# Performance work log

Hardware: AMD Instinct MI355X
Metric: run time of the kernel (lower is better)

The kernel has to match this reference:

```python
import jax, jax.numpy as jnp
import numpy as np
import math

N, LQ, D, H, L, P, DFF, NL = 16, 300, 256, 8, 3, 4, 1024, 6
TLENS = (4096, 2048, 1024)
T = sum(TLENS)
TEMP = 10000.0

def _ln(x, g, b, eps=1e-5):
    m = x.mean(-1, keepdims=True)
    v = ((x - m) ** 2).mean(-1, keepdims=True)
    return (x - m) * jax.lax.rsqrt(v + eps) * g + b

def _mlp2(x, w0, b0, w1, b1):
    return jax.nn.relu(x @ w0.T + b0) @ w1.T + b1

def _sine_embed(ref):
    # ref: (N, LQ, 2) (center, width) -> (N, LQ, 2*D)
    dim_t = TEMP ** (2.0 * (jnp.arange(D) // 2) / D)
    p = ref * (2.0 * math.pi)
    def inter(v):
        return jnp.stack([jnp.sin(v[..., 0::2]), jnp.cos(v[..., 1::2])], -1).reshape(v.shape[:-1] + (-1,))
    pc = p[..., 0:1] / dim_t
    pw = p[..., 1:2] / dim_t
    return jnp.concatenate([inter(pc), inter(pw)], -1)

def _mha(q, k, v, in_w, in_b, out_w, out_b):
    Nb, Lq, Dm = q.shape
    Dh = Dm // H
    wq, wk, wv = jnp.split(in_w, 3, 0)
    bq, bk, bv = jnp.split(in_b, 3, 0)
    qh = (q @ wq.T + bq).reshape(Nb, Lq, H, Dh)
    kh = (k @ wk.T + bk).reshape(Nb, Lq, H, Dh)
    vh = (v @ wv.T + bv).reshape(Nb, Lq, H, Dh)
    att = jax.nn.softmax(jnp.einsum('nqhd,nkhd->nhqk', qh, kh) / math.sqrt(Dh), -1)
    o = jnp.einsum('nhqk,nkhd->nqhd', att, vh).reshape(Nb, Lq, Dm)
    return o @ out_w.T + out_b

def _deform_attn(q, ref, src, pad_mask, t_lens, start, ow, ob, aww, awb, vw, vb, pw, pb):
    # q: (N,LQ,D); ref: (N,LQ,L,2) normalized (center,width); src: (N,T,D)
    Nb, Lq, Dm = q.shape
    Dh = Dm // H
    val = (src @ vw.T + vb) * (~pad_mask)[..., None]
    val = val.reshape(Nb, -1, H, Dh).transpose(0, 2, 1, 3)  # (N,H,T,Dh)
    off = (q @ ow.T + ob).reshape(Nb, Lq, H, L, P)
    aw = jax.nn.softmax((q @ aww.T + awb).reshape(Nb, Lq, H, L * P), -1).reshape(Nb, Lq, H, L, P)
    # 1-D deformable sampling locations: center + offset/P * width * 0.5
    loc = ref[:, :, None, :, 0, None] + off / P * ref[:, :, None, :, 1, None] * 0.5  # (N,LQ,H,L,P)
    tl = t_lens[None, None, None, :, None]
    x = loc * tl.astype(loc.dtype) - 0.5  # align_corners=False linear sampling
    x0f = jnp.floor(x)
    f = x - x0f
    x0 = x0f.astype(jnp.int32)
    m0 = (x0 >= 0) & (x0 < tl)
    m1 = (x0 + 1 >= 0) & (x0 + 1 < tl)
    st = start[None, None, None, :, None]
    i0 = st + jnp.clip(x0, 0, tl - 1)
    i1 = st + jnp.clip(x0 + 1, 0, tl - 1)
    def tr(a):
        return a.transpose(0, 2, 1, 3, 4).reshape(Nb, H, Lq * L * P)
    g0 = jnp.take_along_axis(val, tr(i0)[..., None], axis=2)  # (N,H,M,Dh)
    g1 = jnp.take_along_axis(val, tr(i1)[..., None], axis=2)
    samp = g0 * ((1.0 - tr(f)) * tr(m0))[..., None] + g1 * (tr(f) * tr(m1))[..., None]
    samp = samp.reshape(Nb, H, Lq, L * P, Dh)
    w = tr(aw).reshape(Nb, H, Lq, L * P)
    o = jnp.einsum('nhqk,nhqkd->nqhd', w, samp).reshape(Nb, Lq, Dm)
    return o @ pw.T + pb

def _forward(tgt, enc_output_segments, feature_durations, src, src_valid_ratios,
             grid_w0, grid_b0, grid_w1, grid_b1, qs_w0, qs_b0, qs_w1, qs_b1,
             sa_in_w, sa_in_b, sa_out_w, sa_out_b,
             n1_g, n1_b, n2_g, n2_b, n3_g, n3_b,
             off_w, off_b, aw_w, aw_b, val_w, val_b, outp_w, outp_b,
             ffn_w1, ffn_b1, ffn_w2, ffn_b2,
             temporal_lens, level_start_index, src_padding_mask):
    seg = jax.lax.stop_gradient(enc_output_segments)  # original detaches proposals
    ref = jnp.stack([seg[..., 0], jnp.exp(seg[..., 1])], -1)  # (N,LQ,2) center,width
    out = tgt
    for l in range(NL):
        ref_in = (ref / feature_durations[:, None, None])[:, :, None, :] * src_valid_ratios[:, None, :, None]
        sine = _sine_embed(ref)
        raw_qpos = _mlp2(sine, grid_w0, grid_b0, grid_w1, grid_b1)
        qpos = _mlp2(out, qs_w0, qs_b0, qs_w1, qs_b1) * raw_qpos
        q = out + qpos
        out = _ln(out + _mha(q, q, out, sa_in_w[l], sa_in_b[l], sa_out_w[l], sa_out_b[l]), n1_g[l], n1_b[l])
        ca = _deform_attn(out + qpos, ref_in, src, src_padding_mask, temporal_lens, level_start_index,
                          off_w[l], off_b[l], aw_w[l], aw_b[l], val_w[l], val_b[l], outp_w[l], outp_b[l])
        out = _ln(out + ca, n2_g[l], n2_b[l])
        ff = jax.nn.relu(out @ ffn_w1[l].T + ffn_b1[l]) @ ffn_w2[l].T + ffn_b2[l]
        out = _ln(out + ff, n3_g[l], n3_b[l])
    return out

def setup_inputs():
    key = jax.random.key(0)
    ks = iter(jax.random.split(key, 64))
    def nrm(shape, s=0.02):
        return (s * jax.random.normal(next(ks), shape)).astype(jnp.float32)
    dur = 64.0
    inp = {}
    inp['tgt'] = nrm((N, LQ, D), 1.0)
    c = jax.random.uniform(next(ks), (N, LQ)) * dur
    w = jnp.log(jax.random.uniform(next(ks), (N, LQ)) * 4.0 + 0.5)
    inp['enc_output_segments'] = jnp.stack([c, w], -1)
    inp['feature_durations'] = jnp.full((N,), dur, jnp.float32)
    inp['src'] = nrm((N, T, D), 1.0)
    inp['temporal_lens'] = jnp.array(TLENS, jnp.int32)
    inp['level_start_index'] = jnp.array(np.cumsum((0,) + TLENS[:-1]), jnp.int32)
    inp['src_valid_ratios'] = jnp.ones((N, L), jnp.float32)
    inp['src_padding_mask'] = jnp.zeros((N, T), bool)
    inp['grid_w0'] = nrm((D, 2 * D)); inp['grid_b0'] = jnp.zeros((D,))
    inp['grid_w1'] = nrm((D, D)); inp['grid_b1'] = jnp.zeros((D,))
    inp['qs_w0'] = nrm((D, D)); inp['qs_b0'] = jnp.zeros((D,))
    inp['qs_w1'] = nrm((D, D)); inp['qs_b1'] = jnp.zeros((D,))
    inp['sa_in_w'] = nrm((NL, 3 * D, D)); inp['sa_in_b'] = jnp.zeros((NL, 3 * D))
    inp['sa_out_w'] = nrm((NL, D, D)); inp['sa_out_b'] = jnp.zeros((NL, D))
    for nm in ('n1', 'n2', 'n3'):
        inp[nm + '_g'] = jnp.ones((NL, D)); inp[nm + '_b'] = jnp.zeros((NL, D))
    inp['off_w'] = nrm((NL, H * L * P, D))
    inp['off_b'] = (jax.random.uniform(next(ks), (NL, H * L * P)) * 2.0 - 1.0) * P
    inp['aw_w'] = nrm((NL, H * L * P, D)); inp['aw_b'] = jnp.zeros((NL, H * L * P))
    inp['val_w'] = nrm((NL, D, D)); inp['val_b'] = jnp.zeros((NL, D))
    inp['outp_w'] = nrm((NL, D, D)); inp['outp_b'] = jnp.zeros((NL, D))
    inp['ffn_w1'] = nrm((NL, DFF, D)); inp['ffn_b1'] = jnp.zeros((NL, DFF))
    inp['ffn_w2'] = nrm((NL, D, DFF)); inp['ffn_b2'] = jnp.zeros((NL, D))
    return inp

def reference(tgt, enc_output_segments, feature_durations, src, temporal_lens, level_start_index,
              src_valid_ratios, src_padding_mask,
              grid_w0, grid_b0, grid_w1, grid_b1, qs_w0, qs_b0, qs_w1, qs_b1,
              sa_in_w, sa_in_b, sa_out_w, sa_out_b,
              n1_g, n1_b, n2_g, n2_b, n3_g, n3_b,
              off_w, off_b, aw_w, aw_b, val_w, val_b, outp_w, outp_b,
              ffn_w1, ffn_b1, ffn_w2, ffn_b2):
    return _forward(tgt, enc_output_segments, feature_durations, src, src_valid_ratios,
                    grid_w0, grid_b0, grid_w1, grid_b1, qs_w0, qs_b0, qs_w1, qs_b1,
                    sa_in_w, sa_in_b, sa_out_w, sa_out_b,
                    n1_g, n1_b, n2_g, n2_b, n3_g, n3_b,
                    off_w, off_b, aw_w, aw_b, val_w, val_b, outp_w, outp_b,
                    ffn_w1, ffn_b1, ffn_w2, ffn_b2,
                    temporal_lens, level_start_index, src_padding_mask)
```

## Files before the change

kernel.cpp:

```cpp
#include <hip/hip_runtime.h>
#include <cstdint>

#define NB   16
#define LQN  300
#define DM   256
#define NH   8
#define DH   32
#define NLV  3
#define DFFN 1024
#define NLAY 6
#define TT   7168
#define MROW (NB*LQN)
#define SROW (NB*TT)

typedef __attribute__((ext_vector_type(8))) short bf16x8;
typedef __attribute__((ext_vector_type(4))) float f32x4;

__device__ __forceinline__ float bf2f(short u) {
  unsigned x = ((unsigned)(unsigned short)u) << 16;
  return __builtin_bit_cast(float, x);
}
__device__ __forceinline__ short f2bf(float f) {
  unsigned u = __builtin_bit_cast(unsigned, f);
  u += 0x7fffu + ((u >> 16) & 1u);
  return (short)(u >> 16);
}
__device__ __forceinline__ void load_lds16(const void* g, void* l) {
  __builtin_amdgcn_global_load_lds(
      (const __attribute__((address_space(1))) unsigned int*)g,
      (__attribute__((address_space(3))) unsigned int*)l, 16, 0, 0);
}
#define MFMA(a,b,c) __builtin_amdgcn_mfma_f32_16x16x32_bf16((a),(b),(c),0,0,0)

struct CvtPtrs { const float* p[13]; };

__global__ __launch_bounds__(256)
void cvt_all_kernel(CvtPtrs ptrs, short* __restrict__ dst)
{
  const long gid = (long)blockIdx.x*256 + threadIdx.x;
  const long cums[14] = {0,32768,49152,65536,81920,376832,475136,512000,
                         548864,647168,745472,1138688,1531904,8871936};
  int s = 0;
  #pragma unroll
  for (int i = 1; i < 13; ++i) s += (gid >= cums[i]) ? 1 : 0;
  const long rel = gid - cums[s];
  const float4 v = ((const float4*)ptrs.p[s])[rel];
  long dstIdx = gid;
  if (s == 6) { const long l = rel/6144, w = rel%6144; dstIdx = 475136 + l*12288 + w; }
  else if (s == 7) { const long l = rel/6144, w = rel%6144; dstIdx = 475136 + l*12288 + 6144 + w; }
  ((short4*)dst)[dstIdx] = make_short4(f2bf(v.x), f2bf(v.y), f2bf(v.z), f2bf(v.w));
}

#define VLS 264

__global__ __launch_bounds__(512, 2)
void val_gemm(const short* __restrict__ srcbf, const short* __restrict__ Bw,
              const float* __restrict__ bias, short* __restrict__ Cb,
              const unsigned char* __restrict__ rowmask)
{
  __shared__ short Bs[128*VLS];
  const int tid = threadIdx.x, wid = tid >> 6, lane = tid & 63;
  const int fr = lane & 15, fq = lane >> 4;
  const int coff = blockIdx.y * 128;

  for (int t = tid; t < 4096; t += 512) {
    const int row = t >> 5, ch = t & 31;
    const int chs = ch ^ ((row >> 4) & 7);
    *(bf16x8*)&Bs[row*VLS + chs*8] = *(const bf16x8*)(Bw + (long)(coff + row)*256 + ch*8);
  }
  __syncthreads();

  float bv[8];
  #pragma unroll
  for (int j = 0; j < 2; ++j)
    *(float4*)&bv[j*4] = *(const float4*)(bias + coff + fr*8 + j*4);

  const int rbase = (blockIdx.x*8 + wid) * 32;

  bf16x8 ac0, ac1, an0, an1;
  ac0 = *(const bf16x8*)(srcbf + (long)(rbase + fr)*256 + fq*8);
  ac1 = *(const bf16x8*)(srcbf + (long)(rbase + 16 + fr)*256 + fq*8);

  f32x4 acc[2][8] = {};
  #pragma unroll
  for (int ks = 0; ks < 8; ++ks) {
    if (ks < 7) {
      an0 = *(const bf16x8*)(srcbf + (long)(rbase + fr)*256 + (ks+1)*32 + fq*8);
      an1 = *(const bf16x8*)(srcbf + (long)(rbase + 16 + fr)*256 + (ks+1)*32 + fq*8);
    }
    #pragma unroll
    for (int nt = 0; nt < 8; ++nt) {
      const int row = fr*8 + nt;
      const bf16x8 b = *(const bf16x8*)&Bs[row*VLS + (((ks*4 + fq) ^ ((row >> 4) & 7)))*8];
      acc[0][nt] = MFMA(ac0, b, acc[0][nt]);
      acc[1][nt] = MFMA(ac1, b, acc[1][nt]);
    }
    if (ks < 7) { ac0 = an0; ac1 = an1; }
  }

  #pragma unroll
  for (int h = 0; h < 2; ++h) {
    #pragma unroll
    for (int r = 0; r < 4; ++r) {
      const int grow = rbase + h*16 + fq*4 + r;
      const float msc = rowmask[grow] ? 0.0f : 1.0f;
      bf16x8 o;
      #pragma unroll
      for (int j = 0; j < 8; ++j) o[j] = f2bf((acc[h][j][r] + bv[j]) * msc);
      *(bf16x8*)(Cb + (long)grow*256 + coff + fr*8) = o;
    }
  }
}

template<int EPI>
__global__ __launch_bounds__(256)
void gemm64(const short* __restrict__ A, const short* __restrict__ B,
            const float* __restrict__ bias, const float* __restrict__ bias2,
            float* __restrict__ Cf, short* __restrict__ Cb, short* __restrict__ Cb2,
            int M, int N, int K, int ldc,
            const float* __restrict__ rawq, const float* __restrict__ resid)
{
  __shared__ short As[2][64*64];
  __shared__ short Bs[2][64*64];
  const int tid = threadIdx.x, wid = tid >> 6, lane = tid & 63;
  const int wr = wid >> 1, wc = wid & 1;
  const int fr = lane & 15, fq = lane >> 4;
  const int bm = blockIdx.x, bn = blockIdx.y;
  const int lrow = lane >> 3;
  const int schk = ((lane & 7) ^ lrow) * 8;
  const int nk = K >> 6;

  f32x4 acc[2][2] = {};

  auto stg = [&](int kt, int bsel) {
    const int k0 = kt << 6;
    #pragma unroll
    for (int i = 0; i < 2; ++i) {
      const int rr = wid*16 + i*8 + lrow;
      load_lds16(A + (long)(bm*64 + rr)*K + k0 + schk, &As[bsel][(wid*16 + i*8)*64]);
      load_lds16(B + (long)(bn*64 + rr)*K + k0 + schk, &Bs[bsel][(wid*16 + i*8)*64]);
    }
  };

  stg(0, 0);
  for (int t = 0; t < nk; ++t) {
    const int cur = t & 1;
    if (t + 1 < nk) {
      stg(t + 1, cur ^ 1);
      asm volatile("s_waitcnt vmcnt(4)" ::: "memory");
    } else {
      asm volatile("s_waitcnt vmcnt(0)" ::: "memory");
    }
    __builtin_amdgcn_s_barrier();
    __builtin_amdgcn_sched_barrier(0);
    #pragma unroll
    for (int kk = 0; kk < 64; kk += 32) {
      bf16x8 af[2], bv[2];
      #pragma unroll
      for (int mi = 0; mi < 2; ++mi)
        af[mi] = *(const bf16x8*)&As[cur][(wr*32 + mi*16 + fr)*64 + (((kk>>3)+fq) ^ (fr&7))*8];
      #pragma unroll
      for (int ni = 0; ni < 2; ++ni)
        bv[ni] = *(const bf16x8*)&Bs[cur][(wc*32 + ni*16 + fr)*64 + (((kk>>3)+fq) ^ (fr&7))*8];
      #pragma unroll
      for (int mi = 0; mi < 2; ++mi)
        #pragma unroll
        for (int ni = 0; ni < 2; ++ni)
          acc[mi][ni] = MFMA(af[mi], bv[ni], acc[mi][ni]);
    }
    __builtin_amdgcn_s_barrier();
  }

  #pragma unroll
  for (int mi = 0; mi < 2; ++mi) {
    #pragma unroll
    for (int r = 0; r < 4; ++r) {
      const int grow = bm*64 + wr*32 + mi*16 + fq*4 + r;
      #pragma unroll
      for (int ni = 0; ni < 2; ++ni) {
        const int gcol = bn*64 + wc*32 + ni*16 + fr;
        float v = acc[mi][ni][r];
        if (EPI == 4) v += (gcol < 96) ? bias[gcol] : bias2[gcol-96];
        else v += bias[gcol];
        const long off = (long)grow*ldc + gcol;
        if (EPI == 0) {
          if (Cf) Cf[off] = v;
          if (Cb) Cb[off] = f2bf(v);
        } else if (EPI == 1) {
          Cb[off] = f2bf(fmaxf(v, 0.0f));
        } else if (EPI == 2) {
          const float qp = v * rawq[off];
          Cf[off] = qp;
          Cb[off] = f2bf(resid[off] + qp);
        } else if (EPI == 4) {
          Cf[off] = v;
        }
      }
    }
  }
}

__global__ __launch_bounds__(256)
void ew0_kernel(const float* __restrict__ tgt, float* __restrict__ out, short* __restrict__ outbf)
{
  const long i = (long)blockIdx.x*256 + threadIdx.x;
  const float4 v = ((const float4*)tgt)[i];
  ((float4*)out)[i] = v;
  ((short4*)outbf)[i] = make_short4(f2bf(v.x), f2bf(v.y), f2bf(v.z), f2bf(v.w));
}

__global__ __launch_bounds__(256)
void init_ref_kernel(const float* __restrict__ seg, const float* __restrict__ dur,
                     const float* __restrict__ valid,
                     short* __restrict__ sinebf, float* __restrict__ refin)
{
  const int m = blockIdx.x;
  const int n = m / LQN;
  const int t = threadIdx.x;
  const float c = seg[(long)m*2 + 0];
  const float w = __expf(seg[(long)m*2 + 1]);
  const float e = (float)(t & ~1) * (1.0f/256.0f);
  const float invdim = __expf(-e * 9.2103403719761836f);
  const float twopi = 6.2831853071795864f;
  const float a0 = c * twopi * invdim;
  const float a1 = w * twopi * invdim;
  const float v0 = (t & 1) ? cosf(a0) : sinf(a0);
  const float v1 = (t & 1) ? cosf(a1) : sinf(a1);
  sinebf[(long)m*512 + t]       = f2bf(v0);
  sinebf[(long)m*512 + 256 + t] = f2bf(v1);
  if (t < 6) {
    const int l = t >> 1, cc = t & 1;
    const float rv = cc ? w : c;
    refin[(long)m*6 + l*2 + cc] = rv / dur[n] * valid[n*NLV + l];
  }
}

#define KPAD 320
#define KSTR 40
#define VSTR 328
#define PSTR 328

__global__ __launch_bounds__(256)
void attn_mfma(const short* __restrict__ qk, const short* __restrict__ vv,
               short* __restrict__ outb)
{
  __shared__ short Kl[KPAD*KSTR];
  __shared__ short Vt[DH*VSTR];
  __shared__ short Pl[4][16*PSTR];
  const int b = blockIdx.x;
  const int half = b & 1, h = (b >> 1) & 7, n = b >> 4;
  const int tid = threadIdx.x, wid = tid >> 6, lane = tid & 63;
  const int fr = lane & 15, fq = lane >> 4;

  const short* qkn = qk + (long)n*LQN*512;
  const short* vn  = vv + (long)n*LQN*256;

  for (int t = tid; t < KPAD*4; t += 256) {
    const int r = t >> 2, c = t & 3;
    bf16x8 kv = {}, vw = {};
    if (r < LQN) {
      kv = *(const bf16x8*)(qkn + (long)r*512 + 256 + h*32 + c*8);
      vw = *(const bf16x8*)(vn  + (long)r*256 + h*32 + c*8);
    }
    *(bf16x8*)&Kl[r*KSTR + c*8] = kv;
    #pragma unroll
    for (int j = 0; j < 8; ++j) Vt[(c*8+j)*VSTR + r] = vw[j];
  }
  for (int t = tid; t < 4*16*24; t += 256) {
    const int w = t / (16*24), rr = (t / 24) & 15, cc = t % 24;
    Pl[w][rr*PSTR + 304 + cc] = 0;
  }
  __syncthreads();

  const int tlo = half ? 10 : 0, thi = half ? 19 : 10;
  const float scl2 = 0.17677669529663687f * 1.4426950408889634f;

  for (int qt = tlo + wid; qt < thi; qt += 4) {
    const int q0 = qt * 16;
    const int qrow = min(q0 + fr, LQN-1);
    const bf16x8 qf = *(const bf16x8*)(qkn + (long)qrow*512 + h*32 + fq*8);
    f32x4 s[19];
    #pragma unroll
    for (int t = 0; t < 19; ++t) {
      const bf16x8 kf = *(const bf16x8*)&Kl[(t*16+fr)*KSTR + fq*8];
      s[t] = MFMA(qf, kf, ((f32x4){0.f,0.f,0.f,0.f}));
    }
    float mx[4] = {-3e38f,-3e38f,-3e38f,-3e38f};
    #pragma unroll
    for (int t = 0; t < 19; ++t) {
      const bool valid = (t < 18) || (fr < 12);
      #pragma unroll
      for (int r = 0; r < 4; ++r) if (valid) mx[r] = fmaxf(mx[r], s[t][r]);
    }
    #pragma unroll
    for (int r = 0; r < 4; ++r) {
      #pragma unroll
      for (int o = 1; o < 16; o <<= 1) mx[r] = fmaxf(mx[r], __shfl_xor(mx[r], o));
      mx[r] *= scl2;
    }
    float l[4] = {0.f,0.f,0.f,0.f};
    #pragma unroll
    for (int t = 0; t < 19; ++t) {
      const bool valid = (t < 18) || (fr < 12);
      #pragma unroll
      for (int r = 0; r < 4; ++r) {
        const float p = valid ? exp2f(s[t][r]*scl2 - mx[r]) : 0.0f;
        l[r] += p;
        Pl[wid][(fq*4+r)*PSTR + t*16 + fr] = f2bf(p);
      }
    }
    #pragma unroll
    for (int r = 0; r < 4; ++r) {
      #pragma unroll
      for (int o = 1; o < 16; o <<= 1) l[r] += __shfl_xor(l[r], o);
    }
    f32x4 o0 = {}, o1 = {};
    #pragma unroll
    for (int ck = 0; ck < 10; ++ck) {
      const bf16x8 pf = *(const bf16x8*)&Pl[wid][fr*PSTR + ck*32 + fq*8];
      const bf16x8 v0 = *(const bf16x8*)&Vt[fr*VSTR + ck*32 + fq*8];
      const bf16x8 v1 = *(const bf16x8*)&Vt[(16+fr)*VSTR + ck*32 + fq*8];
      o0 = MFMA(pf, v0, o0);
      o1 = MFMA(pf, v1, o1);
    }
    #pragma unroll
    for (int r = 0; r < 4; ++r) {
      const int qq = q0 + fq*4 + r;
      if (qq < LQN) {
        const float inv = 1.0f / l[r];
        outb[((long)(n*LQN+qq))*256 + h*32 + fr]      = f2bf(o0[r]*inv);
        outb[((long)(n*LQN+qq))*256 + h*32 + 16 + fr] = f2bf(o1[r]*inv);
      }
    }
  }
}

__global__ __launch_bounds__(256)
void ln_kernel(const float* __restrict__ resid, const float* __restrict__ delta,
               const float* __restrict__ g, const float* __restrict__ b,
               float* __restrict__ of, short* __restrict__ ob,
               const float* __restrict__ qpos, short* __restrict__ caqb)
{
  const int m = blockIdx.x, c = threadIdx.x;
  const long idx = (long)m*DM + c;
  const float x = resid[idx] + delta[idx];
  float s = x, s2 = x*x;
  #pragma unroll
  for (int o = 1; o < 64; o <<= 1) { s += __shfl_xor(s, o); s2 += __shfl_xor(s2, o); }
  __shared__ float rs[4], rs2[4];
  const int w = c >> 6;
  if ((c & 63) == 0) { rs[w] = s; rs2[w] = s2; }
  __syncthreads();
  s  = rs[0]+rs[1]+rs[2]+rs[3];
  s2 = rs2[0]+rs2[1]+rs2[2]+rs2[3];
  const float mean = s * (1.0f/DM);
  const float var  = s2 * (1.0f/DM) - mean*mean;
  const float y = (x - mean) * rsqrtf(var + 1e-5f) * g[c] + b[c];
  of[idx] = y;
  if (ob) ob[idx] = f2bf(y);
  if (qpos) caqb[idx] = f2bf(y + qpos[idx]);
}

__global__ __launch_bounds__(256)
void sample_kernel(const short* __restrict__ val, int ldv,
                   const float* __restrict__ offaw, const float* __restrict__ refin,
                   const int* __restrict__ tlens, const int* __restrict__ lstart,
                   short* __restrict__ cab)
{
  const int m = blockIdx.x;
  const int n = m / LQN;
  const int tid = threadIdx.x;
  __shared__ int2  lI[96];
  __shared__ float2 lW[96];
  if ((tid & 31) == 0) {
    const int h = tid >> 5;
    const float* row = offaw + (long)m*192;
    float aw[12];
    float mx = -1e30f;
    #pragma unroll
    for (int lp = 0; lp < 12; ++lp) { aw[lp] = row[96 + h*12 + lp]; mx = fmaxf(mx, aw[lp]); }
    float sum = 0.0f;
    #pragma unroll
    for (int lp = 0; lp < 12; ++lp) { aw[lp] = __expf(aw[lp]-mx); sum += aw[lp]; }
    const float invs = 1.0f / sum;
    #pragma unroll
    for (int lp = 0; lp < 12; ++lp) {
      const int l = lp >> 2;
      const int tli = tlens[l];
      const float off = row[h*12 + lp];
      const float loc = refin[(long)m*6 + l*2] + off * 0.25f * refin[(long)m*6 + l*2 + 1] * 0.5f;
      const float x = loc * (float)tli - 0.5f;
      const float x0f = floorf(x);
      const float f = x - x0f;
      const int x0 = (int)x0f;
      const int i0 = lstart[l] + min(max(x0,   0), tli-1);
      const int i1 = lstart[l] + min(max(x0+1, 0), tli-1);
      const float wgt = aw[lp]*invs;
      const float w0 = (x0   >= 0 && x0   < tli) ? wgt*(1.0f-f) : 0.0f;
      const float w1 = (x0+1 >= 0 && x0+1 < tli) ? wgt*f        : 0.0f;
      lI[h*12 + lp] = make_int2(i0, i1);
      lW[h*12 + lp] = make_float2(w0, w1);
    }
  }
  __syncthreads();
  const int h = tid >> 5;
  const short* vb = val + (long)n*TT*ldv;
  float acc = 0.0f;
  #pragma unroll
  for (int lp = 0; lp < 12; ++lp) {
    const int e = h*12 + lp;
    const int2 ii = lI[e];
    const float2 ww = lW[e];
    acc += ww.x * bf2f(vb[(long)ii.x*ldv + tid]) + ww.y * bf2f(vb[(long)ii.y*ldv + tid]);
  }
  cab[(long)m*DM + tid] = f2bf(acc);
}

static inline void g64(hipStream_t st, int epi, const short* A, const short* B,
                       const float* bias, const float* bias2,
                       float* Cf, short* Cb, short* Cb2,
                       int M, int N, int K, int ldc,
                       const float* rawq = nullptr, const float* resid = nullptr)
{
  dim3 g(M/64, N/64), blk(256);
  switch (epi) {
    case 0: gemm64<0><<<g,blk,0,st>>>(A,B,bias,bias2,Cf,Cb,Cb2,M,N,K,ldc,rawq,resid); break;
    case 1: gemm64<1><<<g,blk,0,st>>>(A,B,bias,bias2,Cf,Cb,Cb2,M,N,K,ldc,rawq,resid); break;
    case 2: gemm64<2><<<g,blk,0,st>>>(A,B,bias,bias2,Cf,Cb,Cb2,M,N,K,ldc,rawq,resid); break;
    default:gemm64<4><<<g,blk,0,st>>>(A,B,bias,bias2,Cf,Cb,Cb2,M,N,K,ldc,rawq,resid); break;
  }
}

extern "C" void kernel_launch(void* const* d_in, const int* in_sizes, int n_in,
                              void* d_out, int out_size, void* d_ws, size_t ws_size,
                              hipStream_t stream)
{
  const float* tgt    = (const float*)d_in[0];
  const float* seg    = (const float*)d_in[1];
  const float* dur    = (const float*)d_in[2];
  const float* src    = (const float*)d_in[3];
  const int*   tlens  = (const int*)d_in[4];
  const int*   lstart = (const int*)d_in[5];
  const float* valid  = (const float*)d_in[6];
  const unsigned char* pmask = (const unsigned char*)d_in[7];
  const float* grid_w0 = (const float*)d_in[8];
  const float* grid_b0 = (const float*)d_in[9];
  const float* grid_w1 = (const float*)d_in[10];
  const float* grid_b1 = (const float*)d_in[11];
  const float* qs_w0 = (const float*)d_in[12];
  const float* qs_b0 = (const float*)d_in[13];
  const float* qs_w1 = (const float*)d_in[14];
  const float* qs_b1 = (const float*)d_in[15];
  const float* sa_in_w  = (const float*)d_in[16];
  const float* sa_in_b  = (const float*)d_in[17];
  const float* sa_out_w = (const float*)d_in[18];
  const float* sa_out_b = (const float*)d_in[19];
  const float* n1_g = (const float*)d_in[20];
  const float* n1_b = (const float*)d_in[21];
  const float* n2_g = (const float*)d_in[22];
  const float* n2_b = (const float*)d_in[23];
  const float* n3_g = (const float*)d_in[24];
  const float* n3_b = (const float*)d_in[25];
  const float* off_w = (const float*)d_in[26];
  const float* off_b = (const float*)d_in[27];
  const float* aw_w  = (const float*)d_in[28];
  const float* aw_b  = (const float*)d_in[29];
  const float* val_w = (const float*)d_in[30];
  const float* val_b = (const float*)d_in[31];
  const float* outp_w = (const float*)d_in[32];
  const float* outp_b = (const float*)d_in[33];
  const float* ffn_w1 = (const float*)d_in[34];
  const float* ffn_b1 = (const float*)d_in[35];
  const float* ffn_w2 = (const float*)d_in[36];
  const float* ffn_b2 = (const float*)d_in[37];

  const long W_G0=0, W_G1=131072, W_QS0=196608, W_QS1=262144, W_SAIN=327680,
             W_SAOUT=1507328, W_OFFAW=1900544, W_VAL=2195456,
             W_OUTP=2588672, W_FFN1=2981888, W_FFN2=4554752, W_SRC=6127616;

  char* ws = (char*)d_ws;
  short* wbf    = (short*)(ws + 0);
  short* srcbf  = wbf + W_SRC;
  short* sinebf = (short*)(ws + 70975488);
  short* ghbf   = (short*)(ws + 75890688);
  float* rawq   = (float*)(ws + 78348288);
  float* out    = (float*)(ws + 83263488);
  short* qbf    = (short*)(ws + 88178688);
  short* outbf  = qbf + (long)MROW*DM;
  short* t1bf   = (short*)(ws + 93093888);
  float* qpos   = (float*)(ws + 95551488);
  short* qkbf   = (short*)(ws + 100466688);
  short* vbf    = (short*)(ws + 105381888);
  short* attnbf = (short*)(ws + 107839488);
  float* tmpf   = (float*)(ws + 110297088);
  short* caqb   = (short*)(ws + 115212288);
  float* offaw  = (float*)(ws + 117669888);
  short* cabf   = (short*)(ws + 128729088);
  short* ffnhbf = (short*)(ws + 131186688);
  float* refin  = (float*)(ws + 141017088);
  short* valbf  = (short*)(ws + 141132288);

  CvtPtrs cp;
  cp.p[0]=grid_w0; cp.p[1]=grid_w1; cp.p[2]=qs_w0; cp.p[3]=qs_w1; cp.p[4]=sa_in_w;
  cp.p[5]=sa_out_w; cp.p[6]=off_w; cp.p[7]=aw_w; cp.p[8]=val_w; cp.p[9]=outp_w;
  cp.p[10]=ffn_w1; cp.p[11]=ffn_w2; cp.p[12]=src;
  cvt_all_kernel<<<dim3(34656), dim3(256), 0, stream>>>(cp, wbf);

  ew0_kernel<<<dim3(1200), dim3(256), 0, stream>>>(tgt, out, outbf);
  init_ref_kernel<<<dim3(MROW), dim3(256), 0, stream>>>(seg, dur, valid, sinebf, refin);

  g64(stream, 1, sinebf, wbf + W_G0, grid_b0, nullptr, nullptr, ghbf, nullptr, MROW, 256, 512, 256);
  g64(stream, 0, ghbf,   wbf + W_G1, grid_b1, nullptr, rawq, nullptr, nullptr, MROW, 256, 256, 256);

  for (int l = 0; l < NLAY; ++l) {
    g64(stream, 1, outbf, wbf + W_QS0, qs_b0, nullptr, nullptr, t1bf, nullptr, MROW, 256, 256, 256);
    g64(stream, 2, t1bf,  wbf + W_QS1, qs_b1, nullptr, qpos, qbf, nullptr, MROW, 256, 256, 256,
        rawq, out);
    g64(stream, 0, qbf, wbf + W_SAIN + (long)l*196608, sa_in_b + l*768, nullptr,
        nullptr, qkbf, nullptr, MROW, 512, 256, 512);
    g64(stream, 0, outbf, wbf + W_SAIN + (long)l*196608 + 131072, sa_in_b + l*768 + 512, nullptr,
        nullptr, vbf, nullptr, MROW, 256, 256, 256);
    attn_mfma<<<dim3(256), dim3(256), 0, stream>>>(qkbf, vbf, attnbf);
    g64(stream, 0, attnbf, wbf + W_SAOUT + (long)l*65536, sa_out_b + l*256, nullptr,
        tmpf, nullptr, nullptr, MROW, 256, 256, 256);
    ln_kernel<<<dim3(MROW), dim3(256), 0, stream>>>(out, tmpf, n1_g + l*256, n1_b + l*256,
                                                    out, outbf, qpos, caqb);
    g64(stream, 4, caqb, wbf + W_OFFAW + (long)l*49152, off_b + l*96, aw_b + l*96,
        offaw, nullptr, nullptr, MROW, 192, 256, 192);
    val_gemm<<<dim3(448, 2), dim3(512), 0, stream>>>(
        srcbf, wbf + W_VAL + (long)l*65536, val_b + l*256, valbf, pmask);
    sample_kernel<<<dim3(MROW), dim3(256), 0, stream>>>(
        valbf, 256, offaw, refin, tlens, lstart, cabf);
    g64(stream, 0, cabf, wbf + W_OUTP + (long)l*65536, outp_b + l*256, nullptr,
        tmpf, nullptr, nullptr, MROW, 256, 256, 256);
    ln_kernel<<<dim3(MROW), dim3(256), 0, stream>>>(out, tmpf, n2_g + l*256, n2_b + l*256,
                                                    out, outbf, nullptr, nullptr);
    g64(stream, 1, outbf, wbf + W_FFN1 + (long)l*262144, ffn_b1 + l*1024, nullptr,
        nullptr, ffnhbf, nullptr, MROW, 1024, 256, 1024);
    g64(stream, 0, ffnhbf, wbf + W_FFN2 + (long)l*262144, ffn_b2 + l*256, nullptr,
        tmpf, nullptr, nullptr, MROW, 256, 1024, 256);
    float* of = (l == NLAY-1) ? (float*)d_out : out;
    ln_kernel<<<dim3(MROW), dim3(256), 0, stream>>>(out, tmpf, n3_g + l*256, n3_b + l*256,
                                                    of, outbf, nullptr, nullptr);
  }
}
```

Baseline: 973.0 us.

## Store deformable-attention value projections in FP8 and hoist all layers' value GEMMs

The value projection output is now stored as software-encoded FP8 (e4m3-style) instead of bf16, and the sampling kernel decodes FP8 on gather. All six layers' value GEMMs are launched up front into separate per-layer FP8 buffers, since they depend only on src and weights. This halves the bytes written by the value GEMM and read by the random-access sampler, at the cost of FP8 quantization error and a larger workspace footprint of six value buffers.

```diff
diff --git a/kernel.cpp b/kernel.cpp
--- a/kernel.cpp
+++ b/kernel.cpp
@@ -12,6 +12,7 @@
 #define TT   7168
 #define MROW (NB*LQN)
 #define SROW (NB*TT)
+#define VAL8_STRIDE 29360128L
 
 typedef __attribute__((ext_vector_type(8))) short bf16x8;
 typedef __attribute__((ext_vector_type(4))) float f32x4;
@@ -24,6 +25,27 @@
   unsigned u = __builtin_bit_cast(unsigned, f);
   u += 0x7fffu + ((u >> 16) & 1u);
   return (short)(u >> 16);
+}
+__device__ __forceinline__ unsigned f2fp8(float f) {
+  const unsigned sgn = (__builtin_bit_cast(unsigned, f) >> 31) << 7;
+  float a = fminf(fabsf(f), 448.0f);
+  unsigned x = __builtin_bit_cast(unsigned, a);
+  const int ex = (int)(x >> 23) - 127;
+  unsigned enc;
+  if (ex >= -6) {
+    x += 0x7FFFFu + ((x >> 20) & 1u);
+    enc = (((x >> 23) - 120u) << 3) | ((x >> 20) & 7u);
+  } else {
+    enc = (unsigned)(int)__builtin_rintf(a * 512.0f);
+  }
+  return sgn | enc;
+}
+__device__ __forceinline__ float fp82f(unsigned v) {
+  const unsigned e = (v >> 3) & 15u, m = v & 7u;
+  float r;
+  if (e == 0) r = (float)m * 0.001953125f;
+  else r = __builtin_bit_cast(float, ((e + 120u) << 23) | (m << 20));
+  return (v & 0x80u) ? -r : r;
 }
 __device__ __forceinline__ void load_lds16(const void* g, void* l) {
   __builtin_amdgcn_global_load_lds(
@@ -55,7 +77,7 @@
 
 __global__ __launch_bounds__(512, 2)
 void val_gemm(const short* __restrict__ srcbf, const short* __restrict__ Bw,
-              const float* __restrict__ bias, short* __restrict__ Cb,
+              const float* __restrict__ bias, unsigned char* __restrict__ C8,
               const unsigned char* __restrict__ rowmask)
 {
   __shared__ short Bs[128*VLS];
@@ -104,10 +126,14 @@
     for (int r = 0; r < 4; ++r) {
       const int grow = rbase + h*16 + fq*4 + r;
       const float msc = rowmask[grow] ? 0.0f : 1.0f;
-      bf16x8 o;
-      #pragma unroll
-      for (int j = 0; j < 8; ++j) o[j] = f2bf((acc[h][j][r] + bv[j]) * msc);
-      *(bf16x8*)(Cb + (long)grow*256 + coff + fr*8) = o;
+      unsigned w0 = 0, w1 = 0;
+      #pragma unroll
+      for (int j = 0; j < 4; ++j) {
+        w0 |= f2fp8((acc[h][j][r]   + bv[j])   * msc) << (j*8);
+        w1 |= f2fp8((acc[h][4+j][r] + bv[4+j]) * msc) << (j*8);
+      }
+      uint2 o; o.x = w0; o.y = w1;
+      *(uint2*)(C8 + (long)grow*256 + coff + fr*8) = o;
     }
   }
 }
@@ -362,7 +388,7 @@
 }
 
 __global__ __launch_bounds__(256)
-void sample_kernel(const short* __restrict__ val, int ldv,
+void sample_kernel(const unsigned char* __restrict__ val8,
                    const float* __restrict__ offaw, const float* __restrict__ refin,
                    const int* __restrict__ tlens, const int* __restrict__ lstart,
                    short* __restrict__ cab)
@@ -404,14 +430,14 @@
   }
   __syncthreads();
   const int h = tid >> 5;
-  const short* vb = val + (long)n*TT*ldv;
+  const unsigned char* vb = val8 + (long)n*TT*256;
   float acc = 0.0f;
   #pragma unroll
   for (int lp = 0; lp < 12; ++lp) {
     const int e = h*12 + lp;
     const int2 ii = lI[e];
     const float2 ww = lW[e];
-    acc += ww.x * bf2f(vb[(long)ii.x*ldv + tid]) + ww.y * bf2f(vb[(long)ii.y*ldv + tid]);
+    acc += ww.x * fp82f(vb[(long)ii.x*256 + tid]) + ww.y * fp82f(vb[(long)ii.y*256 + tid]);
   }
   cab[(long)m*DM + tid] = f2bf(acc);
 }
@@ -498,7 +524,7 @@
   short* cabf   = (short*)(ws + 128729088);
   short* ffnhbf = (short*)(ws + 131186688);
   float* refin  = (float*)(ws + 141017088);
-  short* valbf  = (short*)(ws + 141132288);
+  unsigned char* val8 = (unsigned char*)(ws + 141132288);
 
   CvtPtrs cp;
   cp.p[0]=grid_w0; cp.p[1]=grid_w1; cp.p[2]=qs_w0; cp.p[3]=qs_w1; cp.p[4]=sa_in_w;
@@ -508,6 +534,12 @@
 
   ew0_kernel<<<dim3(1200), dim3(256), 0, stream>>>(tgt, out, outbf);
   init_ref_kernel<<<dim3(MROW), dim3(256), 0, stream>>>(seg, dur, valid, sinebf, refin);
+
+  for (int l = 0; l < NLAY; ++l) {
+    val_gemm<<<dim3(448, 2), dim3(512), 0, stream>>>(
+        srcbf, wbf + W_VAL + (long)l*65536, val_b + l*256,
+        val8 + (long)l*VAL8_STRIDE, pmask);
+  }
 
   g64(stream, 1, sinebf, wbf + W_G0, grid_b0, nullptr, nullptr, ghbf, nullptr, MROW, 256, 512, 256);
   g64(stream, 0, ghbf,   wbf + W_G1, grid_b1, nullptr, rawq, nullptr, nullptr, MROW, 256, 256, 256);
@@ -527,10 +559,8 @@
                                                     out, outbf, qpos, caqb);
     g64(stream, 4, caqb, wbf + W_OFFAW + (long)l*49152, off_b + l*96, aw_b + l*96,
         offaw, nullptr, nullptr, MROW, 192, 256, 192);
-    val_gemm<<<dim3(448, 2), dim3(512), 0, stream>>>(
-        srcbf, wbf + W_VAL + (long)l*65536, val_b + l*256, valbf, pmask);
     sample_kernel<<<dim3(MROW), dim3(256), 0, stream>>>(
-        valbf, 256, offaw, refin, tlens, lstart, cabf);
+        val8 + (long)l*VAL8_STRIDE, offaw, refin, tlens, lstart, cabf);
     g64(stream, 0, cabf, wbf + W_OUTP + (long)l*65536, outp_b + l*256, nullptr,
         tmpf, nullptr, nullptr, MROW, 256, 256, 256);
     ln_kernel<<<dim3(MROW), dim3(256), 0, stream>>>(out, tmpf, n2_g + l*256, n2_b + l*256,
```

New measurement: 1.210 ms. +24.4%, slower.
